# Performance work log

Measured on AMD Instinct MI355X. Metric: run time of the kernel, lower is better.

Reference implementation:

```python
import jax, jax.numpy as jnp
import numpy as np

N_NODES = 50000
N_FEAT = 256
N_HID = 32
N_HEADS = 8
N_CLASSES = 32
N_EDGES = 800000
NEG_SLOPE = 0.2  # PyG GATConv default leaky_relu slope


def setup_inputs() -> dict:
    key = jax.random.key(0)
    ks = jax.random.split(key, 10)
    x = jax.random.normal(ks[0], (N_NODES, N_FEAT), dtype=jnp.float32)
    edge_index = jax.random.randint(ks[1], (2, N_EDGES), 0, N_NODES, dtype=jnp.int64)
    s1 = 1.0 / np.sqrt(N_FEAT)
    s2 = 1.0 / np.sqrt(N_HID * N_HEADS)
    W1 = jax.random.normal(ks[2], (N_FEAT, N_HEADS * N_HID), dtype=jnp.float32) * s1
    a_src1 = jax.random.normal(ks[3], (N_HEADS, N_HID), dtype=jnp.float32) * s1
    a_dst1 = jax.random.normal(ks[4], (N_HEADS, N_HID), dtype=jnp.float32) * s1
    b1 = jnp.zeros((N_HEADS * N_HID,), dtype=jnp.float32)
    W2 = jax.random.normal(ks[5], (N_HEADS * N_HID, N_CLASSES), dtype=jnp.float32) * s2
    a_src2 = jax.random.normal(ks[6], (1, N_CLASSES), dtype=jnp.float32) * s2
    a_dst2 = jax.random.normal(ks[7], (1, N_CLASSES), dtype=jnp.float32) * s2
    b2 = jnp.zeros((N_CLASSES,), dtype=jnp.float32)
    return {"x": x, "edge_index": edge_index, "W1": W1, "a_src1": a_src1,
            "a_dst1": a_dst1, "b1": b1, "W2": W2, "a_src2": a_src2,
            "a_dst2": a_dst2, "b2": b2}


def _gat_conv(h, src, dst, n_nodes, W, a_src, a_dst, heads, ch):
    # h: [N, F_in]; returns [N, heads, ch] aggregated per-node features
    z = (h @ W).reshape(n_nodes, heads, ch)           # [N,H,C]
    alpha_src = jnp.einsum('nhc,hc->nh', z, a_src)    # [N,H]
    alpha_dst = jnp.einsum('nhc,hc->nh', z, a_dst)    # [N,H]
    logits = jax.nn.leaky_relu(alpha_src[src] + alpha_dst[dst], NEG_SLOPE)  # [E,H]
    # segment softmax over incoming edges of each dst node
    m = jax.ops.segment_max(logits, dst, num_segments=n_nodes)  # [N,H]
    e = jnp.exp(logits - m[dst])                                 # [E,H]
    denom = jax.ops.segment_sum(e, dst, num_segments=n_nodes)   # [N,H]
    alpha = e / denom[dst]                                       # [E,H]
    msg = z[src] * alpha[:, :, None]                             # [E,H,C]
    return jax.ops.segment_sum(msg, dst, num_segments=n_nodes)  # [N,H,C]


def reference(x, edge_index, W1, a_src1, a_dst1, b1, W2, a_src2, a_dst2, b2):
    n = x.shape[0]
    # PyG GATConv default: add self loops
    loops = jnp.arange(n, dtype=edge_index.dtype)
    src = jnp.concatenate([edge_index[0], loops])
    dst = jnp.concatenate([edge_index[1], loops])
    h1 = _gat_conv(x, src, dst, n, W1, a_src1, a_dst1, N_HEADS, N_HID)
    h1 = h1.reshape(n, N_HEADS * N_HID) + b1          # concat=True
    h1 = jax.nn.elu(h1)
    # dropout is a no-op in eval mode
    h2 = _gat_conv(h1, src, dst, n, W2, a_src2, a_dst2, 1, N_CLASSES)
    out = h2.mean(axis=1) + b2                        # concat=False, heads=1
    return out
```

## Files before the change

kernel.cpp:

```cpp
#include <hip/hip_runtime.h>

#define NNODES 50000
#define NFEAT 256
#define NHID 32
#define NHEADS 8
#define NCLASSES 32
#define NEDGES 800000
#define ETOT (NEDGES + NNODES)
#define NSCAN_BLK 196
#define GEMM1_BLKS 782
#define SCAT_BLKS 3321

typedef __attribute__((ext_vector_type(8))) short short8;
typedef __attribute__((ext_vector_type(4))) float f32x4;

__device__ __forceinline__ void get_edge(const int* __restrict__ ei, int e,
                                         int& s, int& d) {
    if (e < NEDGES) { s = ei[e]; d = ei[NEDGES + e]; }
    else            { s = e - NEDGES; d = s; }
}
__device__ __forceinline__ float lrelu(float x) { return x > 0.f ? x : 0.2f * x; }
__device__ __forceinline__ unsigned short f2bf(float f) {
    unsigned u = __float_as_uint(f);
    unsigned r = u + 0x7fffu + ((u >> 16) & 1u);
    return (unsigned short)(r >> 16);
}
__device__ __forceinline__ float bflo(unsigned u) { return __uint_as_float(u << 16); }
__device__ __forceinline__ float bfhi(unsigned u) { return __uint_as_float(u & 0xffff0000u); }

__global__ void wprep_hist_k(const float* __restrict__ W1, const float* __restrict__ W2,
                             short8* __restrict__ W1frag, short8* __restrict__ W2frag,
                             const int* __restrict__ ei, int* __restrict__ deg,
                             unsigned short* __restrict__ pos) {
    if (blockIdx.x < 36) {
        int idx = blockIdx.x * 256 + threadIdx.x;
        if (idx < 8192) {
            int kc = idx >> 10, r = idx & 1023;
            int nt = r >> 6, lane = r & 63;
            int l16 = lane & 15, quad = lane >> 4;
            int n = nt * 16 + l16, k0 = kc * 32 + quad * 8;
            short8 v;
#pragma unroll
            for (int j = 0; j < 8; ++j) v[j] = (short)f2bf(W1[(k0 + j) * 256 + n]);
            W1frag[idx] = v;
        } else if (idx < 8192 + 1024) {
            int g = idx - 8192;
            int kc = g >> 7, r = g & 127;
            int nt = r >> 6, lane = r & 63;
            int l16 = lane & 15, quad = lane >> 4;
            int n = nt * 16 + l16, k0 = kc * 32 + quad * 8;
            short8 v;
#pragma unroll
            for (int j = 0; j < 8; ++j) v[j] = (short)f2bf(W2[(k0 + j) * 32 + n]);
            W2frag[g] = v;
        }
    } else {
        int e = (blockIdx.x - 36) * 256 + threadIdx.x;
        if (e >= ETOT) return;
        int d = (e < NEDGES) ? ei[NEDGES + e] : (e - NEDGES);
        pos[e] = (unsigned short)atomicAdd(&deg[d], 1);
    }
}

__global__ void scan_part_k(const int* __restrict__ deg, int* __restrict__ row_local,
                            int* __restrict__ bsum) {
    __shared__ int ws[4];
    int t = threadIdx.x, lane = t & 63, wid = t >> 6;
    int idx = blockIdx.x * 256 + t;
    int v = (idx < NNODES) ? deg[idx] : 0;
    int inc = v;
#pragma unroll
    for (int off = 1; off < 64; off <<= 1) {
        int u = __shfl_up(inc, off, 64);
        if (lane >= off) inc += u;
    }
    if (lane == 63) ws[wid] = inc;
    __syncthreads();
    int woff = 0;
#pragma unroll
    for (int j = 0; j < 4; ++j) woff += (j < wid) ? ws[j] : 0;
    if (idx < NNODES) row_local[idx] = woff + inc - v;
    if (t == 255) bsum[blockIdx.x] = woff + inc;
}

__global__ void scan_fix_k(const int* __restrict__ row_local, const int* __restrict__ bsum,
                           int* __restrict__ row_start) {
    __shared__ int ws[4];
    __shared__ int sboff;
    int t = threadIdx.x, lane = t & 63, wid = t >> 6;
    int v = (t < NSCAN_BLK) ? bsum[t] : 0;
    int inc = v;
#pragma unroll
    for (int off = 1; off < 64; off <<= 1) {
        int u = __shfl_up(inc, off, 64);
        if (lane >= off) inc += u;
    }
    if (lane == 63) ws[wid] = inc;
    __syncthreads();
    int woff = 0;
#pragma unroll
    for (int j = 0; j < 4; ++j) woff += (j < wid) ? ws[j] : 0;
    if (t == blockIdx.x) sboff = woff + inc - v;
    __syncthreads();
    int idx = blockIdx.x * 256 + t;
    if (idx < NNODES) row_start[idx] = row_local[idx] + sboff;
    if (idx == 0) row_start[NNODES] = ETOT;
}

__global__ __launch_bounds__(256) void gemm1_scatter_k(
        const float* __restrict__ x, const short8* __restrict__ Wfrag,
        const float* __restrict__ av, const float* __restrict__ bv,
        unsigned short* __restrict__ z1, float* __restrict__ as_, float* __restrict__ ad_,
        const int* __restrict__ ei, const int* __restrict__ row_start,
        const unsigned short* __restrict__ pos, int* __restrict__ csr_src) {
    if (blockIdx.x >= GEMM1_BLKS) {
        int e = (blockIdx.x - GEMM1_BLKS) * 256 + threadIdx.x;
        if (e >= ETOT) return;
        int s, d;
        get_edge(ei, e, s, d);
        csr_src[row_start[d] + (int)pos[e]] = s;
        return;
    }
    int t = threadIdx.x;
    int w = t >> 6, lane = t & 63;
    int quad = lane >> 4, l16 = lane & 15;
    int mA = blockIdx.x * 64 + w * 16 + l16;
    int mAl = min(mA, NNODES - 1);

    const float4* xp = (const float4*)(x + (size_t)mAl * 256);
    short8 xreg[8];
#pragma unroll
    for (int kc = 0; kc < 8; ++kc) {
        float4 a0 = xp[kc * 8 + quad * 2];
        float4 a1 = xp[kc * 8 + quad * 2 + 1];
        short8 af;
        af[0] = (short)f2bf(a0.x); af[1] = (short)f2bf(a0.y);
        af[2] = (short)f2bf(a0.z); af[3] = (short)f2bf(a0.w);
        af[4] = (short)f2bf(a1.x); af[5] = (short)f2bf(a1.y);
        af[6] = (short)f2bf(a1.z); af[7] = (short)f2bf(a1.w);
        xreg[kc] = af;
    }

    f32x4 acc[16];
#pragma unroll
    for (int nt = 0; nt < 16; ++nt) acc[nt] = (f32x4){0.f, 0.f, 0.f, 0.f};

#pragma unroll
    for (int kc = 0; kc < 8; ++kc) {
        short8 af = xreg[kc];
#pragma unroll
        for (int nt = 0; nt < 16; ++nt) {
            short8 bf8 = Wfrag[kc * 1024 + nt * 64 + lane];
            acc[nt] = __builtin_amdgcn_mfma_f32_16x16x32_bf16(af, bf8, acc[nt], 0, 0, 0);
        }
    }
    int mrow0 = blockIdx.x * 64 + w * 16 + quad * 4;
#pragma unroll
    for (int nt = 0; nt < 16; ++nt) {
        int n = nt * 16 + l16;
#pragma unroll
        for (int r = 0; r < 4; ++r) {
            int mr = mrow0 + r;
            if (mr < NNODES) z1[(size_t)mr * 256 + n] = f2bf(acc[nt][r]);
        }
    }
#pragma unroll
    for (int h = 0; h < 8; ++h) {
        float av0 = av[(2 * h) * 16 + l16], av1v = av[(2 * h + 1) * 16 + l16];
        float bv0 = bv[(2 * h) * 16 + l16], bv1v = bv[(2 * h + 1) * 16 + l16];
#pragma unroll
        for (int r = 0; r < 4; ++r) {
            float pa = acc[2 * h][r] * av0 + acc[2 * h + 1][r] * av1v;
            float pb = acc[2 * h][r] * bv0 + acc[2 * h + 1][r] * bv1v;
#pragma unroll
            for (int off = 1; off < 16; off <<= 1) {
                pa += __shfl_xor(pa, off, 64);
                pb += __shfl_xor(pb, off, 64);
            }
            int mr = mrow0 + r;
            if (l16 == 0 && mr < NNODES) { as_[mr * 8 + h] = pa; ad_[mr * 8 + h] = pb; }
        }
    }
}

__global__ __launch_bounds__(256) void gemm2_mfma_k(
        const unsigned short* __restrict__ h1, const short8* __restrict__ Wfrag,
        const float* __restrict__ av, const float* __restrict__ bv,
        unsigned short* __restrict__ z2b, float* __restrict__ as_, float* __restrict__ ad_) {
    int w = threadIdx.x >> 6, lane = threadIdx.x & 63;
    int quad = lane >> 4, l16 = lane & 15;
    int mA = blockIdx.x * 64 + w * 16 + l16;
    int mAl = min(mA, NNODES - 1);

    f32x4 acc[2];
    acc[0] = (f32x4){0.f, 0.f, 0.f, 0.f};
    acc[1] = (f32x4){0.f, 0.f, 0.f, 0.f};
    for (int kc = 0; kc < 8; ++kc) {
        int k0 = kc * 32 + quad * 8;
        short8 af = *(const short8*)(h1 + (size_t)mAl * 256 + k0);
#pragma unroll
        for (int nt = 0; nt < 2; ++nt) {
            short8 bf8 = Wfrag[kc * 128 + nt * 64 + lane];
            acc[nt] = __builtin_amdgcn_mfma_f32_16x16x32_bf16(af, bf8, acc[nt], 0, 0, 0);
        }
    }
    int mrow0 = blockIdx.x * 64 + w * 16 + quad * 4;
    float av0 = av[l16], av1v = av[16 + l16];
    float bv0 = bv[l16], bv1v = bv[16 + l16];
#pragma unroll
    for (int r = 0; r < 4; ++r) {
        int mr = mrow0 + r;
        float pa = acc[0][r] * av0 + acc[1][r] * av1v;
        float pb = acc[0][r] * bv0 + acc[1][r] * bv1v;
#pragma unroll
        for (int off = 1; off < 16; off <<= 1) {
            pa += __shfl_xor(pa, off, 64);
            pb += __shfl_xor(pb, off, 64);
        }
        if (mr < NNODES) {
            z2b[(size_t)mr * 32 + l16] = f2bf(acc[0][r]);
            z2b[(size_t)mr * 32 + 16 + l16] = f2bf(acc[1][r]);
            if (l16 == 0) { as_[mr] = pa; ad_[mr] = pb; }
        }
    }
}

__global__ void agg1_csr_k(const int* __restrict__ row_start, const int* __restrict__ csr_src,
                           const unsigned short* __restrict__ z, const float* __restrict__ as_,
                           const float* __restrict__ ad_, const float* __restrict__ b,
                           unsigned short* __restrict__ h1) {
    int wv = threadIdx.x >> 6, lane = threadIdx.x & 63;
    int d = blockIdx.x * 4 + wv;
    int h = lane >> 3;
    int c0 = lane * 4;
    int e8 = lane & 7;
    float adh = ad_[d * 8 + h];
    int beg = row_start[d], end = row_start[d + 1];
    float sum = 0.f, a0 = 0.f, a1 = 0.f, a2 = 0.f, a3 = 0.f;

    int idx = beg + e8;
    int sv = csr_src[idx < end ? idx : end - 1];
    float myw = __expf(lrelu(as_[sv * 8 + h] + adh));
    myw = (idx < end) ? myw : 0.f;

    for (int i = beg; i < end; i += 8) {
        int idx2 = i + 8 + e8;
        int sv2 = csr_src[idx2 < end ? idx2 : end - 1];
        float myw2 = __expf(lrelu(as_[sv2 * 8 + h] + adh));
        myw2 = (idx2 < end) ? myw2 : 0.f;

        int se[8];
        float we[8];
#pragma unroll
        for (int e = 0; e < 8; ++e) {
            se[e] = __shfl(sv, e, 64);
            we[e] = __shfl(myw, (lane & 56) | e, 64);
        }
        uint2 q[8];
#pragma unroll
        for (int e = 0; e < 8; ++e)
            q[e] = *(const uint2*)(z + (size_t)se[e] * 256 + c0);
#pragma unroll
        for (int e = 0; e < 8; ++e) {
            float wgt = we[e];
            sum += wgt;
            a0 += wgt * bflo(q[e].x);
            a1 += wgt * bfhi(q[e].x);
            a2 += wgt * bflo(q[e].y);
            a3 += wgt * bfhi(q[e].y);
        }
        sv = sv2;
        myw = myw2;
    }
    float inv = 1.f / sum;
    float o0 = a0 * inv + b[c0 + 0];
    float o1 = a1 * inv + b[c0 + 1];
    float o2 = a2 * inv + b[c0 + 2];
    float o3 = a3 * inv + b[c0 + 3];
    o0 = o0 > 0.f ? o0 : expm1f(o0);
    o1 = o1 > 0.f ? o1 : expm1f(o1);
    o2 = o2 > 0.f ? o2 : expm1f(o2);
    o3 = o3 > 0.f ? o3 : expm1f(o3);
    uint2 pk;
    pk.x = (unsigned)f2bf(o0) | ((unsigned)f2bf(o1) << 16);
    pk.y = (unsigned)f2bf(o2) | ((unsigned)f2bf(o3) << 16);
    *(uint2*)(h1 + (size_t)d * 256 + c0) = pk;
}

__global__ void agg2_csr_k(const int* __restrict__ row_start, const int* __restrict__ csr_src,
                           const unsigned short* __restrict__ z2b, const float* __restrict__ as_,
                           const float* __restrict__ ad_, const float* __restrict__ b,
                           float* __restrict__ out) {
    int g = blockIdx.x * 16 + (threadIdx.x >> 4);
    int l = threadIdx.x & 15;
    int lane = threadIdx.x & 63;
    int c0 = l * 2;
    int beg = row_start[g], end = row_start[g + 1];
    float adn = ad_[g];
    int e8 = l & 7;
    int gb = lane & 48;
    float sum = 0.f, a0 = 0.f, a1 = 0.f;
    int i = beg;
    for (; i + 8 <= end; i += 8) {
        int sv = csr_src[i + e8];
        float myw = __expf(lrelu(as_[sv] + adn));
        int se[8];
        float we[8];
#pragma unroll
        for (int e = 0; e < 8; ++e) {
            se[e] = __shfl(sv, gb | e, 64);
            we[e] = __shfl(myw, gb | (8 | e), 64);
        }
        unsigned q[8];
#pragma unroll
        for (int e = 0; e < 8; ++e)
            q[e] = *(const unsigned*)(z2b + (size_t)se[e] * 32 + c0);
#pragma unroll
        for (int e = 0; e < 8; ++e) {
            float wgt = we[e];
            sum += wgt;
            a0 += wgt * bflo(q[e]);
            a1 += wgt * bfhi(q[e]);
        }
    }
    for (; i < end; ++i) {
        int s = csr_src[i];
        float wgt = __expf(lrelu(as_[s] + adn));
        unsigned q = *(const unsigned*)(z2b + (size_t)s * 32 + c0);
        sum += wgt;
        a0 += wgt * bflo(q);
        a1 += wgt * bfhi(q);
    }
    float inv = 1.f / sum;
    float2 o;
    o.x = a0 * inv + b[c0];
    o.y = a1 * inv + b[c0 + 1];
    *(float2*)(out + (size_t)g * 32 + c0) = o;
}

extern "C" void kernel_launch(void* const* d_in, const int* in_sizes, int n_in,
                              void* d_out, int out_size, void* d_ws, size_t ws_size,
                              hipStream_t stream) {
    const float* x   = (const float*)d_in[0];
    const int*   ei  = (const int*)d_in[1];
    const float* W1  = (const float*)d_in[2];
    const float* av1 = (const float*)d_in[3];
    const float* bv1 = (const float*)d_in[4];
    const float* b1  = (const float*)d_in[5];
    const float* W2  = (const float*)d_in[6];
    const float* av2 = (const float*)d_in[7];
    const float* bv2 = (const float*)d_in[8];
    const float* b2  = (const float*)d_in[9];
    float* out = (float*)d_out;

    unsigned short* z1 = (unsigned short*)d_ws;
    unsigned short* h1 = (unsigned short*)((float*)d_ws + 6400000);
    float* as1 = (float*)d_ws + 12800000;
    float* ad1 = as1 + 400000;
    unsigned short* z2b = (unsigned short*)(ad1 + 400000);
    float* as2 = ad1 + 400000 + 800000;
    float* ad2 = as2 + 50000;
    short8* W1frag = (short8*)(ad2 + 50000);
    short8* W2frag = W1frag + 8192;
    int* deg       = (int*)(ad2 + 50000) + 36864;
    int* row_start = deg + 50000;
    int* csr_src   = row_start + 50001;
    int* row_local = csr_src + 850000;
    int* bsum      = row_local + 50000;
    unsigned short* pos = (unsigned short*)z2b;

    hipMemsetAsync(deg, 0, (size_t)50000 * 4, stream);

    wprep_hist_k<<<36 + SCAT_BLKS, 256, 0, stream>>>(W1, W2, W1frag, W2frag, ei, deg, pos);
    scan_part_k<<<NSCAN_BLK, 256, 0, stream>>>(deg, row_local, bsum);
    scan_fix_k<<<NSCAN_BLK, 256, 0, stream>>>(row_local, bsum, row_start);

    gemm1_scatter_k<<<GEMM1_BLKS + SCAT_BLKS, 256, 0, stream>>>(
        x, W1frag, av1, bv1, z1, as1, ad1, ei, row_start, pos, csr_src);
    agg1_csr_k<<<(NNODES + 3) / 4, 256, 0, stream>>>(row_start, csr_src, z1, as1, ad1, b1, h1);

    gemm2_mfma_k<<<(NNODES + 63) / 64, 256, 0, stream>>>(h1, W2frag, av2, bv2, z2b, as2, ad2);
    agg2_csr_k<<<NNODES / 16, 256, 0, stream>>>(row_start, csr_src, z2b, as2, ad2, b2, out);
}
```

Measured before the change: 282.6 us.

## Split GEMM1 into four column blocks and interleave with CSR scatter blocks

The first-layer GEMM is split so each block computes a quarter of the 256 output columns (two heads), which quadruples the GEMM block count and cuts accumulator registers from 16 to 4 fragments. GEMM blocks are interleaved one-to-one with edge-scatter blocks in the fused launch, so memory-bound scatter work runs alongside compute-bound GEMM work. The cost is that each row's x data is loaded and converted to bf16 four times instead of once, which adds global reads.

```diff
diff --git a/kernel.cpp b/kernel.cpp
--- a/kernel.cpp
+++ b/kernel.cpp
@@ -8,8 +8,10 @@
 #define NEDGES 800000
 #define ETOT (NEDGES + NNODES)
 #define NSCAN_BLK 196
-#define GEMM1_BLKS 782
+#define GEMM1_BLKS4 3128
 #define SCAT_BLKS 3321
+#define PAIRED (2 * GEMM1_BLKS4)
+#define G1_GRID (PAIRED + (SCAT_BLKS - GEMM1_BLKS4))
 
 typedef __attribute__((ext_vector_type(8))) short short8;
 typedef __attribute__((ext_vector_type(4))) float f32x4;
@@ -113,18 +115,24 @@
         unsigned short* __restrict__ z1, float* __restrict__ as_, float* __restrict__ ad_,
         const int* __restrict__ ei, const int* __restrict__ row_start,
         const unsigned short* __restrict__ pos, int* __restrict__ csr_src) {
-    if (blockIdx.x >= GEMM1_BLKS) {
-        int e = (blockIdx.x - GEMM1_BLKS) * 256 + threadIdx.x;
+    int bid = blockIdx.x;
+    bool is_gemm;
+    int gid;
+    if (bid < PAIRED) { is_gemm = !(bid & 1); gid = bid >> 1; }
+    else              { is_gemm = false;      gid = GEMM1_BLKS4 + (bid - PAIRED); }
+    if (!is_gemm) {
+        int e = gid * 256 + threadIdx.x;
         if (e >= ETOT) return;
         int s, d;
         get_edge(ei, e, s, d);
         csr_src[row_start[d] + (int)pos[e]] = s;
         return;
     }
+    int rb = gid >> 2, cb = gid & 3;
     int t = threadIdx.x;
     int w = t >> 6, lane = t & 63;
     int quad = lane >> 4, l16 = lane & 15;
-    int mA = blockIdx.x * 64 + w * 16 + l16;
+    int mA = rb * 64 + w * 16 + l16;
     int mAl = min(mA, NNODES - 1);
 
     const float4* xp = (const float4*)(x + (size_t)mAl * 256);
@@ -141,37 +149,38 @@
         xreg[kc] = af;
     }
 
-    f32x4 acc[16];
-#pragma unroll
-    for (int nt = 0; nt < 16; ++nt) acc[nt] = (f32x4){0.f, 0.f, 0.f, 0.f};
+    f32x4 acc[4];
+#pragma unroll
+    for (int j = 0; j < 4; ++j) acc[j] = (f32x4){0.f, 0.f, 0.f, 0.f};
 
 #pragma unroll
     for (int kc = 0; kc < 8; ++kc) {
         short8 af = xreg[kc];
 #pragma unroll
-        for (int nt = 0; nt < 16; ++nt) {
-            short8 bf8 = Wfrag[kc * 1024 + nt * 64 + lane];
-            acc[nt] = __builtin_amdgcn_mfma_f32_16x16x32_bf16(af, bf8, acc[nt], 0, 0, 0);
-        }
-    }
-    int mrow0 = blockIdx.x * 64 + w * 16 + quad * 4;
-#pragma unroll
-    for (int nt = 0; nt < 16; ++nt) {
-        int n = nt * 16 + l16;
+        for (int j = 0; j < 4; ++j) {
+            short8 bf8 = Wfrag[kc * 1024 + (cb * 4 + j) * 64 + lane];
+            acc[j] = __builtin_amdgcn_mfma_f32_16x16x32_bf16(af, bf8, acc[j], 0, 0, 0);
+        }
+    }
+    int mrow0 = rb * 64 + w * 16 + quad * 4;
+#pragma unroll
+    for (int j = 0; j < 4; ++j) {
+        int n = (cb * 4 + j) * 16 + l16;
 #pragma unroll
         for (int r = 0; r < 4; ++r) {
             int mr = mrow0 + r;
-            if (mr < NNODES) z1[(size_t)mr * 256 + n] = f2bf(acc[nt][r]);
-        }
-    }
-#pragma unroll
-    for (int h = 0; h < 8; ++h) {
-        float av0 = av[(2 * h) * 16 + l16], av1v = av[(2 * h + 1) * 16 + l16];
-        float bv0 = bv[(2 * h) * 16 + l16], bv1v = bv[(2 * h + 1) * 16 + l16];
+            if (mr < NNODES) z1[(size_t)mr * 256 + n] = f2bf(acc[j][r]);
+        }
+    }
+#pragma unroll
+    for (int jj = 0; jj < 2; ++jj) {
+        int h = cb * 2 + jj;
+        float av0 = av[(cb * 4 + 2 * jj) * 16 + l16], av1v = av[(cb * 4 + 2 * jj + 1) * 16 + l16];
+        float bv0 = bv[(cb * 4 + 2 * jj) * 16 + l16], bv1v = bv[(cb * 4 + 2 * jj + 1) * 16 + l16];
 #pragma unroll
         for (int r = 0; r < 4; ++r) {
-            float pa = acc[2 * h][r] * av0 + acc[2 * h + 1][r] * av1v;
-            float pb = acc[2 * h][r] * bv0 + acc[2 * h + 1][r] * bv1v;
+            float pa = acc[2 * jj][r] * av0 + acc[2 * jj + 1][r] * av1v;
+            float pb = acc[2 * jj][r] * bv0 + acc[2 * jj + 1][r] * bv1v;
 #pragma unroll
             for (int off = 1; off < 16; off <<= 1) {
                 pa += __shfl_xor(pa, off, 64);
@@ -375,7 +384,7 @@
     scan_part_k<<<NSCAN_BLK, 256, 0, stream>>>(deg, row_local, bsum);
     scan_fix_k<<<NSCAN_BLK, 256, 0, stream>>>(row_local, bsum, row_start);
 
-    gemm1_scatter_k<<<GEMM1_BLKS + SCAT_BLKS, 256, 0, stream>>>(
+    gemm1_scatter_k<<<G1_GRID, 256, 0, stream>>>(
         x, W1frag, av1, bv1, z1, as1, ad1, ei, row_start, pos, csr_src);
     agg1_csr_k<<<(NNODES + 3) / 4, 256, 0, stream>>>(row_start, csr_src, z1, as1, ad1, b1, h1);
 
```

After: 322.4 us. +14.1%, slower.

## Overlap degree histogram with GEMM1 and software-pipeline agg2 edge loads

Applied to the files above, without the earlier changes.

The degree histogram (atomic counting) now runs in the same launch as the first GEMM, and the CSR scatter becomes its own kernel after the scan. Previously the histogram shared a launch with the weight prep and the scatter shared one with the GEMM. This places the atomics alongside compute-heavy GEMM blocks and adds one kernel launch. Separately, the layer-2 aggregation loop prefetches the next 8 edge sources and weights one iteration ahead and handles the tail by masking, which removes the scalar remainder loop at the cost of some wasted lanes on low-degree nodes.

```diff
diff --git a/kernel.cpp b/kernel.cpp
--- a/kernel.cpp
+++ b/kernel.cpp
@@ -28,37 +28,28 @@
 __device__ __forceinline__ float bflo(unsigned u) { return __uint_as_float(u << 16); }
 __device__ __forceinline__ float bfhi(unsigned u) { return __uint_as_float(u & 0xffff0000u); }
 
-__global__ void wprep_hist_k(const float* __restrict__ W1, const float* __restrict__ W2,
-                             short8* __restrict__ W1frag, short8* __restrict__ W2frag,
-                             const int* __restrict__ ei, int* __restrict__ deg,
-                             unsigned short* __restrict__ pos) {
-    if (blockIdx.x < 36) {
-        int idx = blockIdx.x * 256 + threadIdx.x;
-        if (idx < 8192) {
-            int kc = idx >> 10, r = idx & 1023;
-            int nt = r >> 6, lane = r & 63;
-            int l16 = lane & 15, quad = lane >> 4;
-            int n = nt * 16 + l16, k0 = kc * 32 + quad * 8;
-            short8 v;
-#pragma unroll
-            for (int j = 0; j < 8; ++j) v[j] = (short)f2bf(W1[(k0 + j) * 256 + n]);
-            W1frag[idx] = v;
-        } else if (idx < 8192 + 1024) {
-            int g = idx - 8192;
-            int kc = g >> 7, r = g & 127;
-            int nt = r >> 6, lane = r & 63;
-            int l16 = lane & 15, quad = lane >> 4;
-            int n = nt * 16 + l16, k0 = kc * 32 + quad * 8;
-            short8 v;
-#pragma unroll
-            for (int j = 0; j < 8; ++j) v[j] = (short)f2bf(W2[(k0 + j) * 32 + n]);
-            W2frag[g] = v;
-        }
-    } else {
-        int e = (blockIdx.x - 36) * 256 + threadIdx.x;
-        if (e >= ETOT) return;
-        int d = (e < NEDGES) ? ei[NEDGES + e] : (e - NEDGES);
-        pos[e] = (unsigned short)atomicAdd(&deg[d], 1);
+__global__ void wprep_k(const float* __restrict__ W1, const float* __restrict__ W2,
+                        short8* __restrict__ W1frag, short8* __restrict__ W2frag) {
+    int idx = blockIdx.x * 256 + threadIdx.x;
+    if (idx < 8192) {
+        int kc = idx >> 10, r = idx & 1023;
+        int nt = r >> 6, lane = r & 63;
+        int l16 = lane & 15, quad = lane >> 4;
+        int n = nt * 16 + l16, k0 = kc * 32 + quad * 8;
+        short8 v;
+#pragma unroll
+        for (int j = 0; j < 8; ++j) v[j] = (short)f2bf(W1[(k0 + j) * 256 + n]);
+        W1frag[idx] = v;
+    } else if (idx < 8192 + 1024) {
+        int g = idx - 8192;
+        int kc = g >> 7, r = g & 127;
+        int nt = r >> 6, lane = r & 63;
+        int l16 = lane & 15, quad = lane >> 4;
+        int n = nt * 16 + l16, k0 = kc * 32 + quad * 8;
+        short8 v;
+#pragma unroll
+        for (int j = 0; j < 8; ++j) v[j] = (short)f2bf(W2[(k0 + j) * 32 + n]);
+        W2frag[g] = v;
     }
 }
 
@@ -107,18 +98,17 @@
     if (idx == 0) row_start[NNODES] = ETOT;
 }
 
-__global__ __launch_bounds__(256) void gemm1_scatter_k(
+__global__ __launch_bounds__(256) void gemm1_hist_k(
         const float* __restrict__ x, const short8* __restrict__ Wfrag,
         const float* __restrict__ av, const float* __restrict__ bv,
         unsigned short* __restrict__ z1, float* __restrict__ as_, float* __restrict__ ad_,
-        const int* __restrict__ ei, const int* __restrict__ row_start,
-        const unsigned short* __restrict__ pos, int* __restrict__ csr_src) {
+        const int* __restrict__ ei, int* __restrict__ deg,
+        unsigned short* __restrict__ pos) {
     if (blockIdx.x >= GEMM1_BLKS) {
         int e = (blockIdx.x - GEMM1_BLKS) * 256 + threadIdx.x;
         if (e >= ETOT) return;
-        int s, d;
-        get_edge(ei, e, s, d);
-        csr_src[row_start[d] + (int)pos[e]] = s;
+        int d = (e < NEDGES) ? ei[NEDGES + e] : (e - NEDGES);
+        pos[e] = (unsigned short)atomicAdd(&deg[d], 1);
         return;
     }
     int t = threadIdx.x;
@@ -181,6 +171,15 @@
             if (l16 == 0 && mr < NNODES) { as_[mr * 8 + h] = pa; ad_[mr * 8 + h] = pb; }
         }
     }
+}
+
+__global__ void scatter_k(const int* __restrict__ ei, const int* __restrict__ row_start,
+                          const unsigned short* __restrict__ pos, int* __restrict__ csr_src) {
+    int e = blockIdx.x * 256 + threadIdx.x;
+    if (e >= ETOT) return;
+    int s, d;
+    get_edge(ei, e, s, d);
+    csr_src[row_start[d] + (int)pos[e]] = s;
 }
 
 __global__ __launch_bounds__(256) void gemm2_mfma_k(
@@ -300,10 +299,18 @@
     int e8 = l & 7;
     int gb = lane & 48;
     float sum = 0.f, a0 = 0.f, a1 = 0.f;
-    int i = beg;
-    for (; i + 8 <= end; i += 8) {
-        int sv = csr_src[i + e8];
-        float myw = __expf(lrelu(as_[sv] + adn));
+
+    int idx = beg + e8;
+    int sv = csr_src[idx < end ? idx : end - 1];
+    float myw = __expf(lrelu(as_[sv] + adn));
+    myw = (idx < end) ? myw : 0.f;
+
+    for (int i = beg; i < end; i += 8) {
+        int idx2 = i + 8 + e8;
+        int sv2 = csr_src[idx2 < end ? idx2 : end - 1];
+        float myw2 = __expf(lrelu(as_[sv2] + adn));
+        myw2 = (idx2 < end) ? myw2 : 0.f;
+
         int se[8];
         float we[8];
 #pragma unroll
@@ -322,14 +329,8 @@
             a0 += wgt * bflo(q[e]);
             a1 += wgt * bfhi(q[e]);
         }
-    }
-    for (; i < end; ++i) {
-        int s = csr_src[i];
-        float wgt = __expf(lrelu(as_[s] + adn));
-        unsigned q = *(const unsigned*)(z2b + (size_t)s * 32 + c0);
-        sum += wgt;
-        a0 += wgt * bflo(q);
-        a1 += wgt * bfhi(q);
+        sv = sv2;
+        myw = myw2;
     }
     float inv = 1.f / sum;
     float2 o;
@@ -371,12 +372,15 @@
 
     hipMemsetAsync(deg, 0, (size_t)50000 * 4, stream);
 
-    wprep_hist_k<<<36 + SCAT_BLKS, 256, 0, stream>>>(W1, W2, W1frag, W2frag, ei, deg, pos);
+    wprep_k<<<36, 256, 0, stream>>>(W1, W2, W1frag, W2frag);
+
+    gemm1_hist_k<<<GEMM1_BLKS + SCAT_BLKS, 256, 0, stream>>>(
+        x, W1frag, av1, bv1, z1, as1, ad1, ei, deg, pos);
+
     scan_part_k<<<NSCAN_BLK, 256, 0, stream>>>(deg, row_local, bsum);
     scan_fix_k<<<NSCAN_BLK, 256, 0, stream>>>(row_local, bsum, row_start);
-
-    gemm1_scatter_k<<<GEMM1_BLKS + SCAT_BLKS, 256, 0, stream>>>(
-        x, W1frag, av1, bv1, z1, as1, ad1, ei, row_start, pos, csr_src);
+    scatter_k<<<SCAT_BLKS, 256, 0, stream>>>(ei, row_start, pos, csr_src);
+
     agg1_csr_k<<<(NNODES + 3) / 4, 256, 0, stream>>>(row_start, csr_src, z1, as1, ad1, b1, h1);
 
     gemm2_mfma_k<<<(NNODES + 63) / 64, 256, 0, stream>>>(h1, W2frag, av2, bv2, z2b, as2, ad2);
```

Result: faster. 269.4 us (-4.7%).
